# Kernel optimization log

Hardware: AMD Instinct MI355X
Metric: run time of the kernel (lower is better)

Reference implementation:

```python
import jax, jax.numpy as jnp
import numpy as np

N = 50000       # nodes
E = 800000      # edges (avg degree 16)
H2, H1, D_IN = 64, 128, 256
BN_EPS = 1e-5


def setup_inputs() -> dict:
    key = jax.random.key(0)
    ks = jax.random.split(key, 8)
    return {
        "y_features": jax.random.normal(ks[0], (N, H2), dtype=jnp.float32),
        "edge_src": jax.random.randint(ks[1], (E,), 0, N, dtype=jnp.int32),
        "edge_dst": jax.random.randint(ks[2], (E,), 0, N, dtype=jnp.int32),
        "edge_weight": jax.random.uniform(ks[3], (E,), dtype=jnp.float32),
        "W1": jax.random.normal(ks[4], (H2, H1), dtype=jnp.float32) * (1.0 / np.sqrt(H2)),
        "gamma1": jnp.ones((H1,), jnp.float32),
        "beta1": jnp.zeros((H1,), jnp.float32),
        "W2": jax.random.normal(ks[5], (H1, D_IN), dtype=jnp.float32) * (1.0 / np.sqrt(H1)),
        "gamma2": jnp.ones((D_IN,), jnp.float32),
        "beta2": jnp.zeros((D_IN,), jnp.float32),
    }


def _gcn_layer(x, W, src, dst, w):
    # dropout(p=0) -> support = x @ W -> spmm(adj, support) -> ReLU
    support = x @ W                                   # [N, Dout]
    msgs = support[src] * w[:, None]                  # [E, Dout]
    agg = jax.ops.segment_sum(msgs, dst, num_segments=N)
    return jax.nn.relu(agg)


def _batchnorm(h, gamma, beta):
    # BatchNorm1d in training mode: batch stats over nodes, biased variance
    mean = jnp.mean(h, axis=0)
    var = jnp.var(h, axis=0)
    return gamma * (h - mean) * jax.lax.rsqrt(var + BN_EPS) + beta


def reference(y_features, edge_src, edge_dst, edge_weight,
              W1, gamma1, beta1, W2, gamma2, beta2):
    h1 = _gcn_layer(y_features, W1, edge_src, edge_dst, edge_weight)
    h1 = _batchnorm(h1, gamma1, beta1)
    h2 = _gcn_layer(h1, W2, edge_src, edge_dst, edge_weight)
    h2 = _batchnorm(h2, gamma2, beta2)
    return h2
```

## Files before the change

kernel.cpp:

```cpp
#include <hip/hip_runtime.h>

#define NN 50000
#define NE 800000

typedef unsigned short ushort_t;
typedef __attribute__((ext_vector_type(8))) short short8;
typedef __attribute__((ext_vector_type(4))) float f32x4;

constexpr int NB   = (NN + 127) / 128;
constexpr int BCAP = 4096;
constexpr int CH     = 4096;
constexpr int NBLK_E = (NE + CH - 1) / CH;
constexpr int NBLK_M = (NN + 63) / 64;
constexpr int NY4    = NN * 64 / 4;

__device__ __forceinline__ float bf2f(ushort_t u) {
    union { unsigned int i; float f; } v;
    v.i = ((unsigned int)u) << 16;
    return v.f;
}
__device__ __forceinline__ float bf2f_u(unsigned int lo16) {
    union { unsigned int i; float f; } v;
    v.i = lo16 << 16;
    return v.f;
}
__device__ __forceinline__ float hi16_as_f(unsigned int u) {
    union { unsigned int i; float f; } v;
    v.i = u & 0xffff0000u;
    return v.f;
}
__device__ __forceinline__ ushort_t f2bf(float f) {
    union { float f; unsigned int u; } v;
    v.f = f;
    unsigned int r = (v.u + 0x7fffu + ((v.u >> 16) & 1u)) >> 16;
    return (ushort_t)r;
}


__global__ void cvt_all_k(const float* __restrict__ y, const float* __restrict__ W1,
                          const float* __restrict__ W2, ushort_t* __restrict__ ybf,
                          ushort_t* __restrict__ w1t, ushort_t* __restrict__ w2t) {
    int i = blockIdx.x * blockDim.x + threadIdx.x;
    if (i < NY4) {
        float4 v = reinterpret_cast<const float4*>(y)[i];
        ushort4 o;
        o.x = f2bf(v.x); o.y = f2bf(v.y); o.z = f2bf(v.z); o.w = f2bf(v.w);
        reinterpret_cast<ushort4*>(ybf)[i] = o;
    } else if (i < NY4 + 128 * 64) {
        int j = i - NY4;
        int c = j >> 6, k = j & 63;
        w1t[j] = f2bf(W1[k * 128 + c]);
    } else if (i < NY4 + 128 * 64 + 256 * 128) {
        int j = i - NY4 - 128 * 64;
        int c = j >> 7, k = j & 127;
        w2t[j] = f2bf(W2[k * 256 + c]);
    }
}


__global__ void bblk_k(const int* __restrict__ src, const int* __restrict__ dst,
                       const float* __restrict__ w, uint2* __restrict__ tmp,
                       int* __restrict__ cnt, int E) {
    __shared__ int lcnt[NB], lcur[NB];
    __shared__ uint2 rec[CH];
    int b = blockIdx.x, tid = threadIdx.x;
    int e0 = b * CH;
    int ec = min(CH, E - e0);
    for (int i = tid; i < NB; i += 256) lcnt[i] = 0;
    __syncthreads();
    for (int i = tid; i < ec; i += 256)
        atomicAdd(&lcnt[dst[e0 + i] >> 7], 1);
    __syncthreads();
    if (tid == 0) {
        int run = 0;
        for (int q = 0; q < NB; ++q) { lcur[q] = run; run += lcnt[q]; }
    }
    __syncthreads();
    for (int q = tid; q < NB; q += 256)
        cnt[q * NBLK_E + b] = (lcnt[q] << 16) | lcur[q];
    __syncthreads();
    for (int i = tid; i < ec; i += 256) {
        int d = dst[e0 + i];
        int p = atomicAdd(&lcur[d >> 7], 1);
        uint2 r;
        r.x = (unsigned int)src[e0 + i] | ((unsigned int)(d & 127) << 16);
        r.y = ((unsigned int)f2bf(w[e0 + i])) << 16;
        rec[p] = r;
    }
    __syncthreads();
    for (int i = tid; i < ec; i += 256)
        tmp[(size_t)e0 + i] = rec[i];
}

__global__ void bstat_k(const int* __restrict__ cnt, int* __restrict__ btot) {
    __shared__ int red[256];
    int q = blockIdx.x, tid = threadIdx.x;
    int s = (tid < NBLK_E) ? (cnt[q * NBLK_E + tid] >> 16) : 0;
    red[tid] = s;
    __syncthreads();
    for (int off = 128; off > 0; off >>= 1) {
        if (tid < off) red[tid] += red[tid + off];
        __syncthreads();
    }
    if (tid == 0) btot[q] = red[0];
}

__global__ void bsort_k(const uint2* __restrict__ tmp, const int* __restrict__ cnt,
                        const int* __restrict__ btot, int* __restrict__ rp,
                        unsigned int* __restrict__ epack, int n) {
    __shared__ int rstart[NBLK_E + 1], rlofs[NBLK_E], rcnt[NBLK_E];
    __shared__ int c128[128], cur128[128], ex128[128];
    __shared__ int pre[256];
    __shared__ int s_start;
    __shared__ uint2 rec8[BCAP];
    __shared__ unsigned int spk[BCAP];
    int q = blockIdx.x, tid = threadIdx.x;
    int d0 = q * 128;
    {
        int part = 0;
        for (int b = tid; b < q; b += 256) part += btot[b];
        pre[tid] = part;
        __syncthreads();
        for (int off = 128; off > 0; off >>= 1) {
            if (tid < off) pre[tid] += pre[tid + off];
            __syncthreads();
        }
        if (tid == 0) {
            s_start = pre[0];
            if (q == 0) rp[n] = NE;
        }
        __syncthreads();
    }
    int start = s_start;
    for (int b = tid; b < NBLK_E; b += 256) {
        int v = cnt[q * NBLK_E + b];
        rcnt[b]  = v >> 16;
        rlofs[b] = v & 0xffff;
    }
    if (tid < 128) c128[tid] = 0;
    __syncthreads();
    if (tid == 0) {
        int run = 0;
        for (int b = 0; b < NBLK_E; ++b) { rstart[b] = run; run += rcnt[b]; }
        rstart[NBLK_E] = run;
    }
    __syncthreads();
    int total = min(rstart[NBLK_E], BCAP);
    for (int i = tid; i < total; i += 256) {
        int lo = 0, hi = NBLK_E;
        while (hi - lo > 1) {
            int mid = (lo + hi) >> 1;
            if (rstart[mid] <= i) lo = mid; else hi = mid;
        }
        uint2 r = tmp[(size_t)lo * CH + rlofs[lo] + (i - rstart[lo])];
        rec8[i] = r;
        atomicAdd(&c128[(r.x >> 16) & 127], 1);
    }
    __syncthreads();
    if (tid == 0) {
        int run = 0;
        for (int d = 0; d < 128; ++d) { ex128[d] = run; cur128[d] = run; run += c128[d]; }
    }
    __syncthreads();
    if (tid < 128 && d0 + tid < n) rp[d0 + tid] = start + ex128[tid];
    for (int i = tid; i < total; i += 256) {
        uint2 r = rec8[i];
        int p = atomicAdd(&cur128[(r.x >> 16) & 127], 1);
        spk[p] = r.y | (r.x & 0xffffu);
    }
    __syncthreads();
    for (int i = tid; i < total; i += 256)
        epack[start + i] = spk[i];
}


__global__ void spmm1_k(const ushort_t* __restrict__ yb, const int* __restrict__ rp,
                        const unsigned int* __restrict__ ep,
                        ushort_t* __restrict__ t1, int n) {
    int wid  = (blockIdx.x * blockDim.x + threadIdx.x) >> 6;
    int lane = threadIdx.x & 63;
    if (wid >= n) return;
    int beg = rp[wid], end = rp[wid + 1];
    float acc = 0.f;
    int p = beg;
    for (; p + 16 <= end; p += 16) {
        unsigned int m[16];
#pragma unroll
        for (int j = 0; j < 16; ++j) m[j] = ep[p + j];
        ushort_t u[16];
#pragma unroll
        for (int j = 0; j < 16; ++j)
            u[j] = yb[(size_t)(m[j] & 0xffffu) * 64 + lane];
#pragma unroll
        for (int j = 0; j < 16; ++j)
            acc = fmaf(hi16_as_f(m[j]), bf2f(u[j]), acc);
    }
    for (; p + 4 <= end; p += 4) {
        unsigned int m[4];
#pragma unroll
        for (int j = 0; j < 4; ++j) m[j] = ep[p + j];
        ushort_t u[4];
#pragma unroll
        for (int j = 0; j < 4; ++j)
            u[j] = yb[(size_t)(m[j] & 0xffffu) * 64 + lane];
#pragma unroll
        for (int j = 0; j < 4; ++j)
            acc = fmaf(hi16_as_f(m[j]), bf2f(u[j]), acc);
    }
    for (; p < end; ++p) {
        unsigned int m = ep[p];
        acc = fmaf(hi16_as_f(m), bf2f(yb[(size_t)(m & 0xffffu) * 64 + lane]), acc);
    }
    t1[(size_t)wid * 64 + lane] = f2bf(acc);
}

__global__ void spmm2_k(const ushort_t* __restrict__ h1, const int* __restrict__ rp,
                        const unsigned int* __restrict__ ep,
                        const float* __restrict__ colsum1, const float* __restrict__ colsq1,
                        const float* __restrict__ gamma1, const float* __restrict__ beta1,
                        ushort_t* __restrict__ a2, int n) {
    int wid  = (blockIdx.x * blockDim.x + threadIdx.x) >> 6;
    int lane = threadIdx.x & 63;
    if (wid >= n) return;
    int beg = rp[wid], end = rp[wid + 1];
    float a0 = 0.f, a1 = 0.f, wacc = 0.f;
    int p = beg;
    for (; p + 16 <= end; p += 16) {
        unsigned int m[16];
#pragma unroll
        for (int j = 0; j < 16; ++j) m[j] = ep[p + j];
        unsigned int u[16];
#pragma unroll
        for (int j = 0; j < 16; ++j)
            u[j] = *reinterpret_cast<const unsigned int*>(
                h1 + (size_t)(m[j] & 0xffffu) * 128 + lane * 2);
#pragma unroll
        for (int j = 0; j < 16; ++j) {
            float wt = hi16_as_f(m[j]);
            wacc += wt;
            a0 = fmaf(wt, bf2f_u(u[j] & 0xffffu), a0);
            a1 = fmaf(wt, bf2f_u(u[j] >> 16), a1);
        }
    }
    for (; p + 4 <= end; p += 4) {
        unsigned int m[4];
#pragma unroll
        for (int j = 0; j < 4; ++j) m[j] = ep[p + j];
        unsigned int u[4];
#pragma unroll
        for (int j = 0; j < 4; ++j)
            u[j] = *reinterpret_cast<const unsigned int*>(
                h1 + (size_t)(m[j] & 0xffffu) * 128 + lane * 2);
#pragma unroll
        for (int j = 0; j < 4; ++j) {
            float wt = hi16_as_f(m[j]);
            wacc += wt;
            a0 = fmaf(wt, bf2f_u(u[j] & 0xffffu), a0);
            a1 = fmaf(wt, bf2f_u(u[j] >> 16), a1);
        }
    }
    for (; p < end; ++p) {
        unsigned int m = ep[p];
        float wt = hi16_as_f(m);
        wacc += wt;
        unsigned int u = *reinterpret_cast<const unsigned int*>(
            h1 + (size_t)(m & 0xffffu) * 128 + lane * 2);
        a0 = fmaf(wt, bf2f_u(u & 0xffffu), a0);
        a1 = fmaf(wt, bf2f_u(u >> 16), a1);
    }
    float2 cs = *reinterpret_cast<const float2*>(colsum1 + lane * 2);
    float2 cq = *reinterpret_cast<const float2*>(colsq1 + lane * 2);
    float2 g  = *reinterpret_cast<const float2*>(gamma1 + lane * 2);
    float2 be = *reinterpret_cast<const float2*>(beta1 + lane * 2);
    float m0 = cs.x * (1.0f / NN);
    float v0 = cq.x * (1.0f / NN) - m0 * m0;
    float sc0 = g.x * rsqrtf(v0 + 1e-5f);
    float bi0 = be.x - m0 * sc0;
    float m1 = cs.y * (1.0f / NN);
    float v1 = cq.y * (1.0f / NN) - m1 * m1;
    float sc1 = g.y * rsqrtf(v1 + 1e-5f);
    float bi1 = be.y - m1 * sc1;
    unsigned int o = (unsigned int)f2bf(fmaf(a0, sc0, wacc * bi0))
                   | ((unsigned int)f2bf(fmaf(a1, sc1, wacc * bi1)) << 16);
    *reinterpret_cast<unsigned int*>(a2 + (size_t)wid * 128 + lane * 2) = o;
}


template <int K>
__launch_bounds__(256, 4)
__global__ void mgemm_k(const ushort_t* __restrict__ A, const ushort_t* __restrict__ BT,
                        ushort_t* __restrict__ Cout, float* __restrict__ psum,
                        float* __restrict__ psq, int n, int N) {
    constexpr int K2 = K * 2;
    __shared__ char As[64 * K2];
    __shared__ float lsum[128], lsq[128];
    int tid = threadIdx.x;
    int r0  = blockIdx.x * 64;
    int c0  = blockIdx.y * 128;

    if (tid < 128) { lsum[tid] = 0.f; lsq[tid] = 0.f; }

    {
        const char* Ab = (const char*)(A + (size_t)r0 * K);
#pragma unroll
        for (int it = 0; it < (64 * K2) / 4096; ++it) {
            int p   = (it * 256 + tid) * 16;
            int row = p / K2;
            int cb  = p - row * K2;
            short8 v = *reinterpret_cast<const short8*>(Ab + p);
            *reinterpret_cast<short8*>(As + row * K2 + (cb ^ ((row & 7) << 4))) = v;
        }
    }

    int lane = tid & 63;
    int w    = tid >> 6;
    int wm0  = (w >> 1) * 32;
    int wn0  = (w & 1) * 64;
    int kg   = lane >> 4;
    int lr   = lane & 15;

    short8 bfrag[K / 32][4];
#pragma unroll
    for (int fn = 0; fn < 4; ++fn) {
        const ushort_t* bp = BT + (size_t)(c0 + wn0 + fn * 16 + lr) * K + kg * 8;
#pragma unroll
        for (int ks = 0; ks < K / 32; ++ks)
            bfrag[ks][fn] = *reinterpret_cast<const short8*>(bp + ks * 32);
    }

    __syncthreads();

    f32x4 acc[2][4];
#pragma unroll
    for (int i = 0; i < 2; ++i)
#pragma unroll
        for (int j = 0; j < 4; ++j) acc[i][j] = f32x4{0.f, 0.f, 0.f, 0.f};

#pragma unroll
    for (int ks = 0; ks < K / 32; ++ks) {
        int boff = ks * 64 + kg * 16;
        int row0 = wm0 + lr;
        int row1 = wm0 + 16 + lr;
        short8 a0 = *reinterpret_cast<const short8*>(As + row0 * K2 + (boff ^ ((row0 & 7) << 4)));
        short8 a1 = *reinterpret_cast<const short8*>(As + row1 * K2 + (boff ^ ((row1 & 7) << 4)));
#pragma unroll
        for (int fn = 0; fn < 4; ++fn) {
            acc[0][fn] = __builtin_amdgcn_mfma_f32_16x16x32_bf16(a0, bfrag[ks][fn], acc[0][fn], 0, 0, 0);
            acc[1][fn] = __builtin_amdgcn_mfma_f32_16x16x32_bf16(a1, bfrag[ks][fn], acc[1][fn], 0, 0, 0);
        }
    }

    float s_c[4] = {0.f, 0.f, 0.f, 0.f};
    float q_c[4] = {0.f, 0.f, 0.f, 0.f};
#pragma unroll
    for (int fm = 0; fm < 2; ++fm) {
        int rowb = r0 + wm0 + fm * 16 + kg * 4;
#pragma unroll
        for (int i = 0; i < 4; ++i) {
            int r = rowb + i;
            if (r < n) {
#pragma unroll
                for (int fn = 0; fn < 4; ++fn) {
                    float v = fmaxf(acc[fm][fn][i], 0.f);
                    s_c[fn] += v;
                    q_c[fn] += v * v;
                    int c = c0 + wn0 + fn * 16 + lr;
                    Cout[(size_t)r * N + c] = f2bf(v);
                }
            }
        }
    }
#pragma unroll
    for (int fn = 0; fn < 4; ++fn) {
        float s = s_c[fn], q = q_c[fn];
        s += __shfl_xor(s, 16); q += __shfl_xor(q, 16);
        s += __shfl_xor(s, 32); q += __shfl_xor(q, 32);
        if (lane < 16) {
            int c = wn0 + fn * 16 + lane;
            atomicAdd(&lsum[c], s);
            atomicAdd(&lsq[c], q);
        }
    }
    __syncthreads();
    if (tid < 128) {
        psum[(size_t)blockIdx.x * N + c0 + tid] = lsum[tid];
        psq [(size_t)blockIdx.x * N + c0 + tid] = lsq[tid];
    }
}


template <int F>
__global__ void red_k(const float* __restrict__ psum, const float* __restrict__ psq,
                      float* __restrict__ colsum, float* __restrict__ colsq, int nblk) {
    constexpr int RG = 256 / F;
    __shared__ float ls[256], lq[256];
    int tid = threadIdx.x;
    int c   = tid & (F - 1);
    int rg  = tid / F;
    float s = 0.f, q = 0.f;
    for (int b = blockIdx.x * RG + rg; b < nblk; b += gridDim.x * RG) {
        s += psum[(size_t)b * F + c];
        q += psq [(size_t)b * F + c];
    }
    ls[tid] = s; lq[tid] = q;
    __syncthreads();
    if (tid < F) {
#pragma unroll
        for (int g = 1; g < RG; ++g) { s += ls[g * F + tid]; q += lq[g * F + tid]; }
        atomicAdd(&colsum[tid], s);
        atomicAdd(&colsq[tid], q);
    }
}

__global__ void norm_out_k(const ushort_t* __restrict__ h2, float* __restrict__ out,
                           const float* __restrict__ colsum2, const float* __restrict__ colsq2,
                           const float* __restrict__ gamma2, const float* __restrict__ beta2,
                           int n8) {
    int i = blockIdx.x * blockDim.x + threadIdx.x;
    int stride = gridDim.x * blockDim.x;
    int c = (i * 8) & 255;
    float4 s0, s1, b0, b1;
    {
        float sc[8], bi[8];
#pragma unroll
        for (int j = 0; j < 8; ++j) {
            float m = colsum2[c + j] * (1.0f / NN);
            float v = colsq2[c + j] * (1.0f / NN) - m * m;
            float s = gamma2[c + j] * rsqrtf(v + 1e-5f);
            sc[j] = s;
            bi[j] = beta2[c + j] - m * s;
        }
        s0 = float4{sc[0], sc[1], sc[2], sc[3]};
        s1 = float4{sc[4], sc[5], sc[6], sc[7]};
        b0 = float4{bi[0], bi[1], bi[2], bi[3]};
        b1 = float4{bi[4], bi[5], bi[6], bi[7]};
    }
    for (; i < n8; i += stride) {
        short8 v = reinterpret_cast<const short8*>(h2)[i];
        float4 o0, o1;
        o0.x = fmaf(bf2f((ushort_t)v[0]), s0.x, b0.x);
        o0.y = fmaf(bf2f((ushort_t)v[1]), s0.y, b0.y);
        o0.z = fmaf(bf2f((ushort_t)v[2]), s0.z, b0.z);
        o0.w = fmaf(bf2f((ushort_t)v[3]), s0.w, b0.w);
        o1.x = fmaf(bf2f((ushort_t)v[4]), s1.x, b1.x);
        o1.y = fmaf(bf2f((ushort_t)v[5]), s1.y, b1.y);
        o1.z = fmaf(bf2f((ushort_t)v[6]), s1.z, b1.z);
        o1.w = fmaf(bf2f((ushort_t)v[7]), s1.w, b1.w);
        reinterpret_cast<float4*>(out)[i * 2 + 0] = o0;
        reinterpret_cast<float4*>(out)[i * 2 + 1] = o1;
    }
}


extern "C" void kernel_launch(void* const* d_in, const int* in_sizes, int n_in,
                              void* d_out, int out_size, void* d_ws, size_t ws_size,
                              hipStream_t stream) {
    const float* y      = (const float*)d_in[0];
    const int*   esrc   = (const int*)d_in[1];
    const int*   edst   = (const int*)d_in[2];
    const float* ew     = (const float*)d_in[3];
    const float* W1     = (const float*)d_in[4];
    const float* gamma1 = (const float*)d_in[5];
    const float* beta1  = (const float*)d_in[6];
    const float* W2     = (const float*)d_in[7];
    const float* gamma2 = (const float*)d_in[8];
    const float* beta2  = (const float*)d_in[9];
    float* out = (float*)d_out;

    char* ws = (char*)d_ws;
    size_t off = 0;
    auto alloc = [&](size_t bytes) -> void* {
        void* p = (void*)(ws + off);
        off += (bytes + 255) & ~(size_t)255;
        return p;
    };
    ushort_t* ybf  = (ushort_t*)alloc((size_t)NN * 64 * 2);
    ushort_t* t1   = (ushort_t*)alloc((size_t)NN * 64 * 2);
    ushort_t* h1   = (ushort_t*)alloc((size_t)NN * 128 * 2);
    ushort_t* a2   = (ushort_t*)alloc((size_t)NN * 128 * 2);
    ushort_t* h2   = (ushort_t*)alloc((size_t)NN * 256 * 2);
    ushort_t* w1t  = (ushort_t*)alloc(128 * 64 * 2);
    ushort_t* w2t  = (ushort_t*)alloc(256 * 128 * 2);
    int*   rp      = (int*)alloc((NN + 1) * 4);
    unsigned int* epack = (unsigned int*)alloc((size_t)NE * 4);
    uint2* tmp8    = (uint2*)alloc((size_t)NE * 8);
    int*   cnt     = (int*)alloc((size_t)NB * NBLK_E * 4);
    int*   btot    = (int*)alloc(NB * 4);
    float* psum1   = (float*)alloc((size_t)NBLK_M * 128 * 4);
    float* psq1    = (float*)alloc((size_t)NBLK_M * 128 * 4);
    float* psum2   = (float*)alloc((size_t)NBLK_M * 256 * 4);
    float* psq2    = (float*)alloc((size_t)NBLK_M * 256 * 4);
    float* stats   = (float*)alloc(768 * 4);
    float* colsum1 = stats;
    float* colsq1  = stats + 128;
    float* colsum2 = stats + 256;
    float* colsq2  = stats + 512;
    (void)alloc(64 * 1024);

    hipMemsetAsync(stats, 0, 768 * 4, stream);

    cvt_all_k<<<(NY4 + 128 * 64 + 256 * 128 + 255) / 256, 256, 0, stream>>>(
        y, W1, W2, ybf, w1t, w2t);

    bblk_k<<<NBLK_E, 256, 0, stream>>>(esrc, edst, ew, tmp8, cnt, NE);
    bstat_k<<<NB, 256, 0, stream>>>(cnt, btot);
    bsort_k<<<NB, 256, 0, stream>>>(tmp8, cnt, btot, rp, epack, NN);

    spmm1_k<<<(NN + 3) / 4, 256, 0, stream>>>(ybf, rp, epack, t1, NN);
    mgemm_k<64><<<dim3(NBLK_M, 1), 256, 0, stream>>>(
        t1, w1t, h1, psum1, psq1, NN, 128);
    red_k<128><<<64, 256, 0, stream>>>(psum1, psq1, colsum1, colsq1, NBLK_M);

    spmm2_k<<<(NN + 3) / 4, 256, 0, stream>>>(h1, rp, epack, colsum1, colsq1,
                                              gamma1, beta1, a2, NN);
    mgemm_k<128><<<dim3(NBLK_M, 2), 256, 0, stream>>>(
        a2, w2t, h2, psum2, psq2, NN, 256);
    red_k<256><<<64, 256, 0, stream>>>(psum2, psq2, colsum2, colsq2, NBLK_M);

    norm_out_k<<<2048, 256, 0, stream>>>(h2, out, colsum2, colsq2, gamma2, beta2,
                                         NN * 256 / 8);
}
```

Before: 166.0 us.

## Fuse layer-1 SpMM gather with MFMA GEMM, ReLU and column stats

Replaces the separate spmm1 kernel and the 64-wide mgemm launch with a single kernel. Each block gathers 64 node rows into swizzled LDS, multiplies by W1 with bf16 MFMA, applies ReLU, writes h1 and emits per-block sum/sumsq partials. This removes the t1 round trip through global memory and one launch. In exchange, each wave now processes 16 nodes serially and the unroll drops from 16 to 8, which lowers memory-level parallelism in the gather and may expose latency.

Result: slower. 196.1 us (+18.1%).

```diff
diff --git a/kernel.cpp b/kernel.cpp
--- a/kernel.cpp
+++ b/kernel.cpp
@@ -174,45 +174,124 @@
 }
 
 
-__global__ void spmm1_k(const ushort_t* __restrict__ yb, const int* __restrict__ rp,
-                        const unsigned int* __restrict__ ep,
-                        ushort_t* __restrict__ t1, int n) {
-    int wid  = (blockIdx.x * blockDim.x + threadIdx.x) >> 6;
-    int lane = threadIdx.x & 63;
-    if (wid >= n) return;
-    int beg = rp[wid], end = rp[wid + 1];
-    float acc = 0.f;
-    int p = beg;
-    for (; p + 16 <= end; p += 16) {
-        unsigned int m[16];
-#pragma unroll
-        for (int j = 0; j < 16; ++j) m[j] = ep[p + j];
-        ushort_t u[16];
-#pragma unroll
-        for (int j = 0; j < 16; ++j)
-            u[j] = yb[(size_t)(m[j] & 0xffffu) * 64 + lane];
-#pragma unroll
-        for (int j = 0; j < 16; ++j)
-            acc = fmaf(hi16_as_f(m[j]), bf2f(u[j]), acc);
-    }
-    for (; p + 4 <= end; p += 4) {
-        unsigned int m[4];
-#pragma unroll
-        for (int j = 0; j < 4; ++j) m[j] = ep[p + j];
-        ushort_t u[4];
-#pragma unroll
-        for (int j = 0; j < 4; ++j)
-            u[j] = yb[(size_t)(m[j] & 0xffffu) * 64 + lane];
-#pragma unroll
-        for (int j = 0; j < 4; ++j)
-            acc = fmaf(hi16_as_f(m[j]), bf2f(u[j]), acc);
-    }
-    for (; p < end; ++p) {
-        unsigned int m = ep[p];
-        acc = fmaf(hi16_as_f(m), bf2f(yb[(size_t)(m & 0xffffu) * 64 + lane]), acc);
-    }
-    t1[(size_t)wid * 64 + lane] = f2bf(acc);
-}
+__launch_bounds__(256, 4)
+__global__ void fused1_k(const ushort_t* __restrict__ yb, const int* __restrict__ rp,
+                         const unsigned int* __restrict__ ep,
+                         const ushort_t* __restrict__ BT, ushort_t* __restrict__ h1,
+                         float* __restrict__ psum, float* __restrict__ psq, int n) {
+    constexpr int K = 64, K2 = 128;
+    __shared__ char As[64 * K2];
+    __shared__ float lsum[128], lsq[128];
+    int tid  = threadIdx.x;
+    int r0   = blockIdx.x * 64;
+    int lane = tid & 63;
+    int w    = tid >> 6;
+    int wm0  = (w >> 1) * 32;
+    int wn0  = (w & 1) * 64;
+    int kg   = lane >> 4;
+    int lr   = lane & 15;
+
+    if (tid < 128) { lsum[tid] = 0.f; lsq[tid] = 0.f; }
+
+    short8 bfrag[2][4];
+#pragma unroll
+    for (int fn = 0; fn < 4; ++fn) {
+        const ushort_t* bp = BT + (size_t)(wn0 + fn * 16 + lr) * K + kg * 8;
+#pragma unroll
+        for (int ks = 0; ks < 2; ++ks)
+            bfrag[ks][fn] = *reinterpret_cast<const short8*>(bp + ks * 32);
+    }
+
+#pragma unroll 1
+    for (int nn = 0; nn < 16; ++nn) {
+        int row  = w * 16 + nn;
+        int node = r0 + row;
+        float acc = 0.f;
+        if (node < n) {
+            int beg = rp[node], end = rp[node + 1];
+            int p = beg;
+            for (; p + 8 <= end; p += 8) {
+                unsigned int m[8];
+#pragma unroll
+                for (int j = 0; j < 8; ++j) m[j] = ep[p + j];
+                ushort_t u[8];
+#pragma unroll
+                for (int j = 0; j < 8; ++j)
+                    u[j] = yb[(size_t)(m[j] & 0xffffu) * 64 + lane];
+#pragma unroll
+                for (int j = 0; j < 8; ++j)
+                    acc = fmaf(hi16_as_f(m[j]), bf2f(u[j]), acc);
+            }
+            for (; p < end; ++p) {
+                unsigned int m = ep[p];
+                acc = fmaf(hi16_as_f(m), bf2f(yb[(size_t)(m & 0xffffu) * 64 + lane]), acc);
+            }
+        }
+        int off  = lane * 2;
+        int addr = row * K2 + (((off & 0x70) ^ ((row & 7) << 4)) | (off & 0xF));
+        *reinterpret_cast<ushort_t*>(As + addr) = f2bf(acc);
+    }
+
+    __syncthreads();
+
+    f32x4 acc[2][4];
+#pragma unroll
+    for (int i = 0; i < 2; ++i)
+#pragma unroll
+        for (int j = 0; j < 4; ++j) acc[i][j] = f32x4{0.f, 0.f, 0.f, 0.f};
+
+#pragma unroll
+    for (int ks = 0; ks < 2; ++ks) {
+        int boff = ks * 64 + kg * 16;
+        int row0 = wm0 + lr;
+        int row1 = wm0 + 16 + lr;
+        short8 a0 = *reinterpret_cast<const short8*>(As + row0 * K2 + (boff ^ ((row0 & 7) << 4)));
+        short8 a1 = *reinterpret_cast<const short8*>(As + row1 * K2 + (boff ^ ((row1 & 7) << 4)));
+#pragma unroll
+        for (int fn = 0; fn < 4; ++fn) {
+            acc[0][fn] = __builtin_amdgcn_mfma_f32_16x16x32_bf16(a0, bfrag[ks][fn], acc[0][fn], 0, 0, 0);
+            acc[1][fn] = __builtin_amdgcn_mfma_f32_16x16x32_bf16(a1, bfrag[ks][fn], acc[1][fn], 0, 0, 0);
+        }
+    }
+
+    float s_c[4] = {0.f, 0.f, 0.f, 0.f};
+    float q_c[4] = {0.f, 0.f, 0.f, 0.f};
+#pragma unroll
+    for (int fm = 0; fm < 2; ++fm) {
+        int rowb = r0 + wm0 + fm * 16 + kg * 4;
+#pragma unroll
+        for (int i = 0; i < 4; ++i) {
+            int r = rowb + i;
+            if (r < n) {
+#pragma unroll
+                for (int fn = 0; fn < 4; ++fn) {
+                    float v = fmaxf(acc[fm][fn][i], 0.f);
+                    s_c[fn] += v;
+                    q_c[fn] += v * v;
+                    int c = wn0 + fn * 16 + lr;
+                    h1[(size_t)r * 128 + c] = f2bf(v);
+                }
+            }
+        }
+    }
+#pragma unroll
+    for (int fn = 0; fn < 4; ++fn) {
+        float s = s_c[fn], q = q_c[fn];
+        s += __shfl_xor(s, 16); q += __shfl_xor(q, 16);
+        s += __shfl_xor(s, 32); q += __shfl_xor(q, 32);
+        if (lane < 16) {
+            int c = wn0 + fn * 16 + lane;
+            atomicAdd(&lsum[c], s);
+            atomicAdd(&lsq[c], q);
+        }
+    }
+    __syncthreads();
+    if (tid < 128) {
+        psum[(size_t)blockIdx.x * 128 + tid] = lsum[tid];
+        psq [(size_t)blockIdx.x * 128 + tid] = lsq[tid];
+    }
+}
+
 
 __global__ void spmm2_k(const ushort_t* __restrict__ h1, const int* __restrict__ rp,
                         const unsigned int* __restrict__ ep,
@@ -475,7 +554,6 @@
         return p;
     };
     ushort_t* ybf  = (ushort_t*)alloc((size_t)NN * 64 * 2);
-    ushort_t* t1   = (ushort_t*)alloc((size_t)NN * 64 * 2);
     ushort_t* h1   = (ushort_t*)alloc((size_t)NN * 128 * 2);
     ushort_t* a2   = (ushort_t*)alloc((size_t)NN * 128 * 2);
     ushort_t* h2   = (ushort_t*)alloc((size_t)NN * 256 * 2);
@@ -506,9 +584,7 @@
     bstat_k<<<NB, 256, 0, stream>>>(cnt, btot);
     bsort_k<<<NB, 256, 0, stream>>>(tmp8, cnt, btot, rp, epack, NN);
 
-    spmm1_k<<<(NN + 3) / 4, 256, 0, stream>>>(ybf, rp, epack, t1, NN);
-    mgemm_k<64><<<dim3(NBLK_M, 1), 256, 0, stream>>>(
-        t1, w1t, h1, psum1, psq1, NN, 128);
+    fused1_k<<<NBLK_M, 256, 0, stream>>>(ybf, rp, epack, w1t, h1, psum1, psq1, NN);
     red_k<128><<<64, 256, 0, stream>>>(psum1, psq1, colsum1, colsq1, NBLK_M);
 
     spmm2_k<<<(NN + 3) / 4, 256, 0, stream>>>(h1, rp, epack, colsum1, colsq1,
```

## Shrink edge bucketing chunks, parallelize serial prefix scans, fold stats memset into convert

Applied to the files above, without the earlier changes.

Cuts the edge chunk size from 4096 to 1024, giving about four times as many bucketing blocks and more parallelism in the first sort pass. The single-thread serial prefix sums in bblk_k and bsort_k are replaced with block-wide Hillis-Steele scans, and bstat_k now loops so it can handle more than 256 chunks. The stats memset is folded into the conversion kernel, removing one launch. The risk is that bsort_k must now scan and gather from more, smaller runs per bucket, which adds fragmented reads.

New measurement: 154.3 us, median of 2. 7.0% less time.

```diff
diff --git a/kernel.cpp b/kernel.cpp
--- a/kernel.cpp
+++ b/kernel.cpp
@@ -9,10 +9,11 @@
 
 constexpr int NB   = (NN + 127) / 128;
 constexpr int BCAP = 4096;
-constexpr int CH     = 4096;
+constexpr int CH     = 1024;
 constexpr int NBLK_E = (NE + CH - 1) / CH;
 constexpr int NBLK_M = (NN + 63) / 64;
 constexpr int NY4    = NN * 64 / 4;
+constexpr int CVT_N  = NY4 + 128 * 64 + 256 * 128 + 768;
 
 __device__ __forceinline__ float bf2f(ushort_t u) {
     union { unsigned int i; float f; } v;
@@ -39,7 +40,8 @@
 
 __global__ void cvt_all_k(const float* __restrict__ y, const float* __restrict__ W1,
                           const float* __restrict__ W2, ushort_t* __restrict__ ybf,
-                          ushort_t* __restrict__ w1t, ushort_t* __restrict__ w2t) {
+                          ushort_t* __restrict__ w1t, ushort_t* __restrict__ w2t,
+                          float* __restrict__ stats) {
     int i = blockIdx.x * blockDim.x + threadIdx.x;
     if (i < NY4) {
         float4 v = reinterpret_cast<const float4*>(y)[i];
@@ -54,6 +56,8 @@
         int j = i - NY4 - 128 * 64;
         int c = j >> 7, k = j & 127;
         w2t[j] = f2bf(W2[k * 256 + c]);
+    } else if (i < CVT_N) {
+        stats[i - (NY4 + 128 * 64 + 256 * 128)] = 0.f;
     }
 }
 
@@ -62,6 +66,7 @@
                        const float* __restrict__ w, uint2* __restrict__ tmp,
                        int* __restrict__ cnt, int E) {
     __shared__ int lcnt[NB], lcur[NB];
+    __shared__ int sm[256];
     __shared__ uint2 rec[CH];
     int b = blockIdx.x, tid = threadIdx.x;
     int e0 = b * CH;
@@ -71,9 +76,22 @@
     for (int i = tid; i < ec; i += 256)
         atomicAdd(&lcnt[dst[e0 + i] >> 7], 1);
     __syncthreads();
-    if (tid == 0) {
-        int run = 0;
-        for (int q = 0; q < NB; ++q) { lcur[q] = run; run += lcnt[q]; }
+    {
+        int i0 = tid * 2;
+        int v0 = (i0 < NB) ? lcnt[i0] : 0;
+        int v1 = (i0 + 1 < NB) ? lcnt[i0 + 1] : 0;
+        int s = v0 + v1;
+        sm[tid] = s;
+        __syncthreads();
+        for (int off = 1; off < 256; off <<= 1) {
+            int x = (tid >= off) ? sm[tid - off] : 0;
+            __syncthreads();
+            sm[tid] += x;
+            __syncthreads();
+        }
+        int excl = sm[tid] - s;
+        if (i0 < NB) lcur[i0] = excl;
+        if (i0 + 1 < NB) lcur[i0 + 1] = excl + v0;
     }
     __syncthreads();
     for (int q = tid; q < NB; q += 256)
@@ -95,7 +113,8 @@
 __global__ void bstat_k(const int* __restrict__ cnt, int* __restrict__ btot) {
     __shared__ int red[256];
     int q = blockIdx.x, tid = threadIdx.x;
-    int s = (tid < NBLK_E) ? (cnt[q * NBLK_E + tid] >> 16) : 0;
+    int s = 0;
+    for (int b = tid; b < NBLK_E; b += 256) s += cnt[q * NBLK_E + b] >> 16;
     red[tid] = s;
     __syncthreads();
     for (int off = 128; off > 0; off >>= 1) {
@@ -116,6 +135,12 @@
     __shared__ unsigned int spk[BCAP];
     int q = blockIdx.x, tid = threadIdx.x;
     int d0 = q * 128;
+    for (int b = tid; b < NBLK_E; b += 256) {
+        int v = cnt[q * NBLK_E + b];
+        rcnt[b]  = v >> 16;
+        rlofs[b] = v & 0xffff;
+    }
+    if (tid < 128) c128[tid] = 0;
     {
         int part = 0;
         for (int b = tid; b < q; b += 256) part += btot[b];
@@ -132,17 +157,27 @@
         __syncthreads();
     }
     int start = s_start;
-    for (int b = tid; b < NBLK_E; b += 256) {
-        int v = cnt[q * NBLK_E + b];
-        rcnt[b]  = v >> 16;
-        rlofs[b] = v & 0xffff;
-    }
-    if (tid < 128) c128[tid] = 0;
-    __syncthreads();
-    if (tid == 0) {
-        int run = 0;
-        for (int b = 0; b < NBLK_E; ++b) { rstart[b] = run; run += rcnt[b]; }
-        rstart[NBLK_E] = run;
+    {
+        int b0 = tid * 4;
+        int w0 = (b0 + 0 < NBLK_E) ? rcnt[b0 + 0] : 0;
+        int w1 = (b0 + 1 < NBLK_E) ? rcnt[b0 + 1] : 0;
+        int w2 = (b0 + 2 < NBLK_E) ? rcnt[b0 + 2] : 0;
+        int w3 = (b0 + 3 < NBLK_E) ? rcnt[b0 + 3] : 0;
+        int s = w0 + w1 + w2 + w3;
+        pre[tid] = s;
+        __syncthreads();
+        for (int off = 1; off < 256; off <<= 1) {
+            int x = (tid >= off) ? pre[tid - off] : 0;
+            __syncthreads();
+            pre[tid] += x;
+            __syncthreads();
+        }
+        int excl = pre[tid] - s;
+        if (b0 + 0 < NBLK_E) rstart[b0 + 0] = excl;
+        if (b0 + 1 < NBLK_E) rstart[b0 + 1] = excl + w0;
+        if (b0 + 2 < NBLK_E) rstart[b0 + 2] = excl + w0 + w1;
+        if (b0 + 3 < NBLK_E) rstart[b0 + 3] = excl + w0 + w1 + w2;
+        if (tid == 255) rstart[NBLK_E] = pre[255];
     }
     __syncthreads();
     int total = min(rstart[NBLK_E], BCAP);
@@ -497,10 +532,7 @@
     float* colsq2  = stats + 512;
     (void)alloc(64 * 1024);
 
-    hipMemsetAsync(stats, 0, 768 * 4, stream);
-
-    cvt_all_k<<<(NY4 + 128 * 64 + 256 * 128 + 255) / 256, 256, 0, stream>>>(
-        y, W1, W2, ybf, w1t, w2t);
+    cvt_all_k<<<(CVT_N + 255) / 256, 256, 0, stream>>>(y, W1, W2, ybf, w1t, w2t, stats);
 
     bblk_k<<<NBLK_E, 256, 0, stream>>>(esrc, edst, ew, tmp8, cnt, NE);
     bstat_k<<<NB, 256, 0, stream>>>(cnt, btot);
```
